# Optimization experiments

Measured on AMD Instinct MI355X. Metric: run time of the kernel, lower is better.

The kernel has to match this reference:

```python
import jax, jax.numpy as jnp
import numpy as np

B, DIM, H, W = 2, 192, 256, 256
WIN = 4
EPS = 1e-5


def _cd_conj(x):
    if len(x) == 1:
        return x
    h = len(x) // 2
    return np.concatenate([_cd_conj(x[:h]), -x[h:]])


def _cd_mult(a, b):
    n = len(a)
    if n == 1:
        return a * b
    h = n // 2
    a1, a2, b1, b2 = a[:h], a[h:], b[:h], b[h:]
    c1 = _cd_mult(a1, b1) - _cd_mult(_cd_conj(b2), a2)
    c2 = _cd_mult(b2, a1) + _cd_mult(a2, _cd_conj(b1))
    return np.concatenate([c1, c2])


def _sedenion_table(n=16):
    # M[i, j, k] = sign s such that e_i * e_j = s * e_k (Cayley-Dickson)
    eye = np.eye(n, dtype=np.float32)
    M = np.zeros((n, n, n), dtype=np.float32)
    for i in range(n):
        for j in range(n):
            M[i, j] = _cd_mult(eye[i], eye[j])
    return M

SED_TABLE = jnp.asarray(_sedenion_table(16))  # (16,16,16)


def layer_norm(x, g, b):
    m = x.mean(-1, keepdims=True)
    v = ((x - m) ** 2).mean(-1, keepdims=True)
    return (x - m) * jax.lax.rsqrt(v + EPS) * g + b


def get_window(x):
    # (B,C,H,W) -> (B,H/4,W/4, s1*s2*C)
    b, c, h, w = x.shape
    x = x.reshape(b, c, h // WIN, WIN, w // WIN, WIN)
    x = x.transpose(0, 2, 4, 3, 5, 1)  # b, h', w', s1, s2, c
    return x.reshape(b, h // WIN, w // WIN, WIN * WIN * c)


def reverse_window(x, c):
    b, hh, ww, _ = x.shape
    x = x.reshape(b, hh, ww, WIN, WIN, c)
    x = x.transpose(0, 5, 1, 3, 2, 4)  # b, c, h', s1, w', s2
    return x.reshape(b, c, hh * WIN, ww * WIN)


def sedenion_full_weight(w_sed):
    # w_sed: (16, dim, dim) component weights -> (16*dim, 16*dim) structured matrix
    d = w_sed.shape[1]
    wf = jnp.einsum('ijk,jde->idke', SED_TABLE, w_sed)
    return wf.reshape(16 * d, 16 * w_sed.shape[2])


def setup_inputs() -> dict:
    key = jax.random.key(0)
    ks = jax.random.split(key, 8)
    d, dh = DIM, 4 * DIM
    s = 0.02
    return {
        'x': jax.random.normal(ks[0], (B, DIM, H, W), jnp.float32),
        'norm1_g': jnp.ones((d,), jnp.float32),
        'norm1_b': jnp.zeros((d,), jnp.float32),
        'w_sed': jax.random.normal(ks[1], (16, d, d), jnp.float32) * s,
        'proj_w': jax.random.normal(ks[2], (d, d), jnp.float32) * s,
        'proj_b': jnp.zeros((d,), jnp.float32),
        'norm2_g': jnp.ones((d,), jnp.float32),
        'norm2_b': jnp.zeros((d,), jnp.float32),
        'fc1_w': jax.random.normal(ks[3], (d, dh), jnp.float32) * s,
        'fc1_b': jnp.zeros((dh,), jnp.float32),
        'fc2_w': jax.random.normal(ks[4], (dh, d), jnp.float32) * s,
        'fc2_b': jnp.zeros((d,), jnp.float32),
    }


def reference(x, norm1_g, norm1_b, w_sed, proj_w, proj_b,
              norm2_g, norm2_b, fc1_w, fc1_b, fc2_w, fc2_b):
    b, c, h, w = x.shape
    # --- attention branch (norm1 -> window -> sedenion linear -> unwindow -> gelu -> proj) ---
    xn = layer_norm(x.transpose(0, 2, 3, 1), norm1_g, norm1_b).transpose(0, 3, 1, 2)
    xw = get_window(xn)                               # (B, H/4, W/4, 16*C)
    wf = sedenion_full_weight(w_sed)                  # (16C, 16C)
    xw = xw @ wf
    x1 = reverse_window(xw, c)                        # (B, C, H, W)
    y = x1.transpose(0, 2, 3, 1)                      # b h w c
    y = jax.nn.gelu(y, approximate=False)
    y = y @ proj_w + proj_b
    x = x + y.transpose(0, 3, 1, 2)
    # --- mlp branch ---
    hbr = layer_norm(x.transpose(0, 2, 3, 1), norm2_g, norm2_b)
    hbr = jax.nn.gelu(hbr @ fc1_w + fc1_b, approximate=False)
    hbr = hbr @ fc2_w + fc2_b
    x = x + hbr.transpose(0, 3, 1, 2)
    return x
```

## Files before the change

### kernel.cpp

```cpp
#include <hip/hip_runtime.h>

typedef short short8 __attribute__((ext_vector_type(8)));
typedef float f32x4 __attribute__((ext_vector_type(4)));

#define DEVINL __device__ __forceinline__

struct SedTab { signed char s[256]; unsigned char j[256]; };

static void cd_mult_host(const float* a, const float* b, float* r, int n) {
    if (n == 1) { r[0] = a[0] * b[0]; return; }
    int h = n / 2;
    float cb1[8], cb2[8], t1[8], t2[8], t3[8], t4[8];
    cb1[0] = b[0]; for (int i = 1; i < h; ++i) cb1[i] = -b[i];
    cb2[0] = b[h]; for (int i = 1; i < h; ++i) cb2[i] = -b[h + i];
    cd_mult_host(a,     b,   t1, h);
    cd_mult_host(cb2,   a+h, t2, h);
    cd_mult_host(b+h,   a,   t3, h);
    cd_mult_host(a+h,   cb1, t4, h);
    for (int i = 0; i < h; ++i) { r[i] = t1[i] - t2[i]; r[h + i] = t3[i] + t4[i]; }
}

static SedTab build_sed() {
    SedTab t{};
    for (int i = 0; i < 16; ++i)
        for (int jj = 0; jj < 16; ++jj) {
            float a[16] = {0}, b[16] = {0}, r[16] = {0};
            a[i] = 1.0f; b[jj] = 1.0f;
            cd_mult_host(a, b, r, 16);
            for (int k = 0; k < 16; ++k)
                if (r[k] != 0.0f) {
                    t.s[i * 16 + k] = (r[k] > 0.f) ? 1 : -1;
                    t.j[i * 16 + k] = (unsigned char)jj;
                }
        }
    return t;
}
static const SedTab g_sed = build_sed();

DEVINL unsigned short f2bf(float v) {
    union { float f; unsigned int u; } c; c.f = v;
    unsigned int r = (c.u + 0x7FFFu + ((c.u >> 16) & 1u)) >> 16;
    return (unsigned short)r;
}
DEVINL float bf2f(unsigned short u) {
    union { unsigned int i; float f; } c; c.i = ((unsigned int)u) << 16; return c.f;
}

DEVINL float gelu_f(float v) {
    float u = 1.5957691216f * (v + 0.044715f * v * v * v);
    return v / (1.0f + __expf(-u));
}

DEVINL void gl2lds16(const void* g, void* l) {
    __builtin_amdgcn_global_load_lds((__attribute__((address_space(1))) const unsigned int*)g,
                                     (__attribute__((address_space(3))) unsigned int*)l, 16, 0, 0);
}

DEVINL int swz(int k, int row) {
    return (k & ~63) | ((((k >> 3) ^ row) & 7) << 3) | (k & 7);
}

__global__ __launch_bounds__(256) void build_wft(const float* __restrict__ w_sed,
                                                 unsigned short* __restrict__ wfT,
                                                 SedTab tab) {
    __shared__ float t[32][33];
    int n0 = blockIdx.y * 32, kk0 = blockIdx.x * 32;
    int k = n0 / 192, i = kk0 / 192;
    int j = tab.j[i * 16 + k];
    float s = (float)tab.s[i * 16 + k];
    int e0 = n0 - k * 192, dd0 = kk0 - i * 192;
    int tx = threadIdx.x & 31, ty = threadIdx.x >> 5;
    const float* base = w_sed + ((size_t)j * 192 + dd0) * 192 + e0;
    for (int it = 0; it < 4; ++it) {
        int row = ty + it * 8;
        t[row][tx] = base[(size_t)row * 192 + tx];
    }
    __syncthreads();
    unsigned short* ob = wfT + (size_t)n0 * 3072 + kk0;
    for (int it = 0; it < 4; ++it) {
        int row = ty + it * 8;
        ob[(size_t)row * 3072 + tx] = f2bf(s * t[tx][row]);
    }
}

__global__ __launch_bounds__(256) void prep_w(const float* __restrict__ proj,
                                              const float* __restrict__ fc1,
                                              const float* __restrict__ fc2,
                                              unsigned short* __restrict__ projT,
                                              unsigned short* __restrict__ fc1T,
                                              unsigned short* __restrict__ fc2T) {
    int t = blockIdx.x * 256 + threadIdx.x;
    if (t < 192 * 192) projT[t] = f2bf(proj[(t % 192) * 192 + t / 192]);
    if (t < 768 * 192) {
        int n = t / 192, k = t % 192;
        fc1T[n * 192 + swz(k, n)] = f2bf(fc1[(size_t)k * 768 + n]);
    }
    if (t < 192 * 768) {
        int o = t / 768, k = t % 768;
        fc2T[o * 768 + swz(k, o)] = f2bf(fc2[(size_t)k * 192 + o]);
    }
}

__global__ __launch_bounds__(256) void ln1_win(const float* __restrict__ x,
                                               const float* __restrict__ g,
                                               const float* __restrict__ bta,
                                               unsigned short* __restrict__ xw,
                                               unsigned short* __restrict__ xwin) {
    __shared__ float vals[192 * 65];
    __shared__ float ps[8][64];
    __shared__ float mrs[2][64];
    int t = threadIdx.x;
    int bid = blockIdx.x;
    int x0 = (bid & 3) << 6;
    int y  = (bid >> 2) & 255;
    int b  = bid >> 10;
    int px = t & 63, cg = t >> 6;
    const float* xp = x + ((size_t)b * 192 * 65536) + (size_t)y * 256 + x0 + px;
    float s = 0.f, s2 = 0.f;
    for (int c = cg; c < 192; c += 4) {
        float v = xp[(size_t)c * 65536];
        vals[c * 65 + px] = v;
        s += v; s2 += v * v;
    }
    ps[cg][px] = s; ps[cg + 4][px] = s2;
    __syncthreads();
    if (t < 64) {
        float S  = ps[0][t] + ps[1][t] + ps[2][t] + ps[3][t];
        float S2 = ps[4][t] + ps[5][t] + ps[6][t] + ps[7][t];
        float mean = S * (1.0f / 192.0f);
        float var  = S2 * (1.0f / 192.0f) - mean * mean;
        mrs[0][t] = mean;
        mrs[1][t] = rsqrtf(var + 1e-5f);
    }
    __syncthreads();
    int wh = y >> 2, wr = y & 3;
    for (int i = t; i < 192 * 64; i += 256) {
        int p = i / 192;
        int c = i - p * 192;
        float v = vals[c * 65 + p];
        int xx = x0 + p;
        int ww = xx >> 2, wc = xx & 3;
        int gp = ((b * 64 + wh) * 64 + ww) * 16 + wr * 4 + wc;
        size_t o = (size_t)gp * 192 + c;
        xwin[o] = f2bf(v);
        xw[o] = f2bf((v - mrs[0][p]) * mrs[1][p] * g[c] + bta[c]);
    }
}

template<int TM, int TN, int EPI>
__global__ __launch_bounds__(256, 2) void gemm_bf16(
        const unsigned short* __restrict__ A, const unsigned short* __restrict__ BT,
        const float* __restrict__ bias, unsigned short* __restrict__ outB,
        unsigned short* __restrict__ xresb,
        const float* __restrict__ g2, const float* __restrict__ b2,
        int K, int N) {
    constexpr int WN = TN / 2;
    constexpr int NT = WN / 16;
    constexpr int MT = TM / 32;
    constexpr int HR = TM / 2;
    __shared__ __align__(16) char smem[(TM * 64 + TN * 64) * 2];
    short* lsA = (short*)smem;
    short* lsB = (short*)(smem + TM * 64 * 2);
    int tid = threadIdx.x, lane = tid & 63, wid = tid >> 6;
    int wrow = wid >> 1, wcol = wid & 1;
    int lm = lane & 15, lq = lane >> 4;
    int bm = blockIdx.x * TM, bn = blockIdx.y * TN;
    const unsigned short* Ag = A + (size_t)bm * K;
    const unsigned short* Bg = BT + (size_t)bn * K;
    f32x4 acc[MT][NT] = {};
    for (int k0 = 0; k0 < K; k0 += 64) {
        #pragma unroll
        for (int it = 0; it < TM / 32; ++it) {
            int p = (it * 4 + wid) * 64 + lane;
            int r = p >> 3;
            int q = (p & 7) ^ (r & 7);
            gl2lds16(Ag + (size_t)r * K + k0 + q * 8, lsA + (it * 4 + wid) * 512);
        }
        #pragma unroll
        for (int it = 0; it < TN / 32; ++it) {
            int p = (it * 4 + wid) * 64 + lane;
            int r = p >> 3;
            int q = (p & 7) ^ (r & 7);
            gl2lds16(Bg + (size_t)r * K + k0 + q * 8, lsB + (it * 4 + wid) * 512);
        }
        __syncthreads();
        #pragma unroll
        for (int s = 0; s < 2; ++s) {
            short8 af[MT], bfr[NT];
            #pragma unroll
            for (int mt = 0; mt < MT; ++mt) {
                int r = wrow * HR + mt * 16 + lm;
                int q = s * 4 + lq;
                int pos = r * 8 + (q ^ (r & 7));
                af[mt] = *(const short8*)&lsA[pos * 8];
            }
            #pragma unroll
            for (int nt = 0; nt < NT; ++nt) {
                int r = wcol * WN + nt * 16 + lm;
                int q = s * 4 + lq;
                int pos = r * 8 + (q ^ (r & 7));
                bfr[nt] = *(const short8*)&lsB[pos * 8];
            }
            #pragma unroll
            for (int mt = 0; mt < MT; ++mt)
                #pragma unroll
                for (int nt = 0; nt < NT; ++nt)
                    acc[mt][nt] = __builtin_amdgcn_mfma_f32_16x16x32_bf16(af[mt], bfr[nt], acc[mt][nt], 0, 0, 0);
        }
        __syncthreads();
    }
    int rowB = bm + wrow * HR + lq * 4;
    int colB = bn + wcol * WN + lm;

    if constexpr (EPI == 0) {
        #pragma unroll
        for (int mt = 0; mt < MT; ++mt)
            #pragma unroll
            for (int nt = 0; nt < NT; ++nt)
                #pragma unroll
                for (int r = 0; r < 4; ++r) {
                    int gr = rowB + mt * 16 + r;
                    int gc = colB + nt * 16;
                    float v = acc[mt][nt][r];
                    if (bias) v += bias[gc];
                    outB[(size_t)gr * N + gc] = f2bf(gelu_f(v));
                }
    } else {
        float sA[MT][4], s2A[MT][4];
        #pragma unroll
        for (int mt = 0; mt < MT; ++mt)
            #pragma unroll
            for (int r = 0; r < 4; ++r) { sA[mt][r] = 0.f; s2A[mt][r] = 0.f; }
        #pragma unroll
        for (int mt = 0; mt < MT; ++mt)
            #pragma unroll
            for (int nt = 0; nt < NT; ++nt)
                #pragma unroll
                for (int r = 0; r < 4; ++r) {
                    int gr = rowB + mt * 16 + r;
                    int gc = colB + nt * 16;
                    size_t o = (size_t)gr * 192 + gc;
                    float v = bf2f(xresb[o]) + acc[mt][nt][r] + bias[gc];
                    xresb[o] = f2bf(v);
                    acc[mt][nt][r] = v;
                    sA[mt][r] += v; s2A[mt][r] += v * v;
                }
        #pragma unroll
        for (int mt = 0; mt < MT; ++mt)
            #pragma unroll
            for (int r = 0; r < 4; ++r)
                #pragma unroll
                for (int msk = 1; msk < 16; msk <<= 1) {
                    sA[mt][r]  += __shfl_xor(sA[mt][r],  msk, 64);
                    s2A[mt][r] += __shfl_xor(s2A[mt][r], msk, 64);
                }
        float* psS   = (float*)smem;
        float* psS2  = psS + 256;
        float* pmean = psS2 + 256;
        float* prsig = pmean + 128;
        if (lm == 0) {
            #pragma unroll
            for (int mt = 0; mt < MT; ++mt)
                #pragma unroll
                for (int r = 0; r < 4; ++r) {
                    int rl = wrow * HR + mt * 16 + lq * 4 + r;
                    psS [rl * 2 + wcol] = sA[mt][r];
                    psS2[rl * 2 + wcol] = s2A[mt][r];
                }
        }
        __syncthreads();
        if (tid < TM) {
            float S  = psS[tid * 2]  + psS[tid * 2 + 1];
            float S2 = psS2[tid * 2] + psS2[tid * 2 + 1];
            float mean = S * (1.0f / 192.0f);
            float var  = S2 * (1.0f / 192.0f) - mean * mean;
            pmean[tid] = mean;
            prsig[tid] = rsqrtf(var + 1e-5f);
        }
        __syncthreads();
        float gw[NT], bw[NT];
        #pragma unroll
        for (int nt = 0; nt < NT; ++nt) {
            int gc = colB + nt * 16;
            gw[nt] = g2[gc]; bw[nt] = b2[gc];
        }
        #pragma unroll
        for (int mt = 0; mt < MT; ++mt)
            #pragma unroll
            for (int nt = 0; nt < NT; ++nt)
                #pragma unroll
                for (int r = 0; r < 4; ++r) {
                    int gr = rowB + mt * 16 + r;
                    int rl = wrow * HR + mt * 16 + lq * 4 + r;
                    int gc = colB + nt * 16;
                    float v = (acc[mt][nt][r] - pmean[rl]) * prsig[rl] * gw[nt] + bw[nt];
                    outB[(size_t)gr * 192 + swz(gc, gr)] = f2bf(v);
                }
    }
}

__global__ __launch_bounds__(256, 2) void ffn_fused(
        const unsigned short* __restrict__ A3, const unsigned short* __restrict__ fc1T,
        const unsigned short* __restrict__ fc2T, const float* __restrict__ b1,
        const float* __restrict__ b2, const unsigned short* __restrict__ xresb,
        float* __restrict__ outF) {
    __shared__ __align__(16) char smem[81920];
    short* A3s = (short*)smem;
    short* wA  = (short*)(smem + 24576);
    short* wB  = (short*)(smem + 49152);
    short* Sb  = (short*)(smem + 73728);
    int tid = threadIdx.x, lane = tid & 63, wid = tid >> 6;
    int wrow = wid >> 1, wcol = wid & 1;
    int lm = lane & 15, lq = lane >> 4;
    int bm = blockIdx.x * 64;

    const unsigned short* A3g = A3 + (size_t)bm * 192;
    #pragma unroll
    for (int it = 0; it < 6; ++it) {
        int ch = (it * 4 + wid) * 64 + lane;
        gl2lds16(A3g + ch * 8, A3s + (it * 4 + wid) * 512);
    }

    f32x4 acc2[2][6] = {};
    for (int nb = 0; nb < 12; ++nb) {
        const unsigned short* f1g = fc1T + (size_t)nb * 64 * 192;
        #pragma unroll
        for (int it = 0; it < 6; ++it) {
            int ch = (it * 4 + wid) * 64 + lane;
            gl2lds16(f1g + ch * 8, wA + (it * 4 + wid) * 512);
        }
        int kb = nb * 64;
        #pragma unroll
        for (int it = 0; it < 6; ++it) {
            int ch = (it * 4 + wid) * 64 + lane;
            gl2lds16(fc2T + (size_t)(ch >> 3) * 768 + kb + (ch & 7) * 8,
                     wB + (it * 4 + wid) * 512);
        }
        __syncthreads();
        f32x4 acc1[2][2] = {};
        #pragma unroll
        for (int ks = 0; ks < 6; ++ks) {
            int c = ks * 4 + lq;
            short8 af[2], bfr[2];
            #pragma unroll
            for (int mt = 0; mt < 2; ++mt) {
                int r = wrow * 32 + mt * 16 + lm;
                int slot = (c & ~7) | ((c ^ r) & 7);
                af[mt] = *(const short8*)&A3s[r * 192 + slot * 8];
            }
            #pragma unroll
            for (int nt = 0; nt < 2; ++nt) {
                int n = wcol * 32 + nt * 16 + lm;
                int slot = (c & ~7) | ((c ^ n) & 7);
                bfr[nt] = *(const short8*)&wA[n * 192 + slot * 8];
            }
            #pragma unroll
            for (int mt = 0; mt < 2; ++mt)
                #pragma unroll
                for (int nt = 0; nt < 2; ++nt)
                    acc1[mt][nt] = __builtin_amdgcn_mfma_f32_16x16x32_bf16(af[mt], bfr[nt], acc1[mt][nt], 0, 0, 0);
        }
        #pragma unroll
        for (int nt = 0; nt < 2; ++nt) {
            int cl = wcol * 32 + nt * 16 + lm;
            float bv = b1[nb * 64 + cl];
            #pragma unroll
            for (int mt = 0; mt < 2; ++mt)
                #pragma unroll
                for (int r = 0; r < 4; ++r) {
                    int row = wrow * 32 + mt * 16 + lq * 4 + r;
                    float v = gelu_f(acc1[mt][nt][r] + bv);
                    int slot = ((cl >> 3) ^ row) & 7;
                    Sb[row * 64 + slot * 8 + (cl & 7)] = f2bf(v);
                }
        }
        __syncthreads();
        #pragma unroll
        for (int ks = 0; ks < 2; ++ks) {
            int c = ks * 4 + lq;
            short8 sf[2], wf[6];
            #pragma unroll
            for (int mt = 0; mt < 2; ++mt) {
                int r = wrow * 32 + mt * 16 + lm;
                int slot = (c ^ r) & 7;
                sf[mt] = *(const short8*)&Sb[r * 64 + slot * 8];
            }
            #pragma unroll
            for (int nt = 0; nt < 6; ++nt) {
                int o = wcol * 96 + nt * 16 + lm;
                int slot = (c ^ o) & 7;
                wf[nt] = *(const short8*)&wB[o * 64 + slot * 8];
            }
            #pragma unroll
            for (int mt = 0; mt < 2; ++mt)
                #pragma unroll
                for (int nt = 0; nt < 6; ++nt)
                    acc2[mt][nt] = __builtin_amdgcn_mfma_f32_16x16x32_bf16(sf[mt], wf[nt], acc2[mt][nt], 0, 0, 0);
        }
        __syncthreads();
    }
    float* T = (float*)smem;
    #pragma unroll
    for (int nt = 0; nt < 6; ++nt) {
        int col = wcol * 96 + nt * 16 + lm;
        float bv = b2[col];
        #pragma unroll
        for (int mt = 0; mt < 2; ++mt)
            #pragma unroll
            for (int r = 0; r < 4; ++r) {
                int row = wrow * 32 + mt * 16 + lq * 4 + r;
                float xr = bf2f(xresb[(size_t)(bm + row) * 192 + col]);
                T[row * 201 + col] = acc2[mt][nt][r] + bv + xr;
            }
    }
    __syncthreads();
    int b  = bm >> 16;
    int wh = (bm >> 10) & 63;
    int ww0 = (bm >> 4) & 63;
    int ybase = wh * 4, xbase = ww0 * 4;
    for (int idx = tid; idx < 3072; idx += 256) {
        int xq = idx & 3, run = idx >> 2;
        int c = run >> 2, wr = run & 3;
        int p = xq * 16 + wr * 4;
        f32x4 val;
        val[0] = T[(p + 0) * 201 + c];
        val[1] = T[(p + 1) * 201 + c];
        val[2] = T[(p + 2) * 201 + c];
        val[3] = T[(p + 3) * 201 + c];
        size_t o = (((size_t)b * 192 + c) * 256 + (ybase + wr)) * 256 + xbase + xq * 4;
        *(f32x4*)&outF[o] = val;
    }
}

extern "C" void kernel_launch(void* const* d_in, const int* in_sizes, int n_in,
                              void* d_out, int out_size, void* d_ws, size_t ws_size,
                              hipStream_t stream) {
    const float* x      = (const float*)d_in[0];
    const float* n1g    = (const float*)d_in[1];
    const float* n1b    = (const float*)d_in[2];
    const float* w_sed  = (const float*)d_in[3];
    const float* proj_w = (const float*)d_in[4];
    const float* proj_b = (const float*)d_in[5];
    const float* n2g    = (const float*)d_in[6];
    const float* n2b    = (const float*)d_in[7];
    const float* fc1_w  = (const float*)d_in[8];
    const float* fc1_b  = (const float*)d_in[9];
    const float* fc2_w  = (const float*)d_in[10];
    const float* fc2_b  = (const float*)d_in[11];
    float* out = (float*)d_out;

    char* ws = (char*)d_ws;
    unsigned short* wfT   = (unsigned short*)(ws);
    unsigned short* xw    = (unsigned short*)(ws + 18874368);
    unsigned short* A2    = (unsigned short*)(ws + 69206016);
    unsigned short* xresb = (unsigned short*)(ws + 119537664);
    unsigned short* projT = (unsigned short*)(ws + 169869312);
    unsigned short* fc1T  = (unsigned short*)(ws + 169943040);
    unsigned short* fc2T  = (unsigned short*)(ws + 170237952);
    unsigned short* A3    = A2;

    build_wft<<<dim3(96, 96), 256, 0, stream>>>(w_sed, wfT, g_sed);
    prep_w<<<576, 256, 0, stream>>>(proj_w, fc1_w, fc2_w, projT, fc1T, fc2T);
    ln1_win<<<2048, 256, 0, stream>>>(x, n1g, n1b, xw, xresb);

    gemm_bf16<128, 128, 0><<<dim3(64, 24), 256, 0, stream>>>(
        xw, wfT, nullptr, A2, nullptr, nullptr, nullptr, 3072, 3072);
    gemm_bf16<128, 192, 3><<<dim3(1024, 1), 256, 0, stream>>>(
        A2, projT, proj_b, A3, xresb, n2g, n2b, 192, 192);
    ffn_fused<<<2048, 256, 0, stream>>>(A3, fc1T, fc2T, fc1_b, fc2_b, xresb, out);
}
```

Measured before the change: 608.4 us.

## Double-buffer fc1 slices and keep A3 tile in registers in fused FFN

The FFN kernel now loads its 64-row activation tile directly from global memory into registers once, rather than staging it in LDS. This frees an LDS region, which is used to double-buffer the fc1 weight slices. fc1 slice nb+2 and fc2 slice nb+1 are now prefetched right after the barriers, so the global-to-LDS copies overlap with the MFMA work of the current slice. The full __syncthreads are replaced by explicit waitcnt plus s_barrier, and s_setprio is raised around the MFMA loops. The cost is more VGPRs for the register-resident A fragments and more delicate hand-written synchronization.

```diff
diff --git a/kernel.cpp b/kernel.cpp
--- a/kernel.cpp
+++ b/kernel.cpp
@@ -305,8 +305,8 @@
         const float* __restrict__ b2, const unsigned short* __restrict__ xresb,
         float* __restrict__ outF) {
     __shared__ __align__(16) char smem[81920];
-    short* A3s = (short*)smem;
-    short* wA  = (short*)(smem + 24576);
+    short* wA0 = (short*)smem;
+    short* wA1 = (short*)(smem + 24576);
     short* wB  = (short*)(smem + 49152);
     short* Sb  = (short*)(smem + 73728);
     int tid = threadIdx.x, lane = tid & 63, wid = tid >> 6;
@@ -315,51 +315,64 @@
     int bm = blockIdx.x * 64;
 
     const unsigned short* A3g = A3 + (size_t)bm * 192;
-    #pragma unroll
-    for (int it = 0; it < 6; ++it) {
-        int ch = (it * 4 + wid) * 64 + lane;
-        gl2lds16(A3g + ch * 8, A3s + (it * 4 + wid) * 512);
-    }
-
-    f32x4 acc2[2][6] = {};
-    for (int nb = 0; nb < 12; ++nb) {
-        const unsigned short* f1g = fc1T + (size_t)nb * 64 * 192;
+
+    auto stage_fc1 = [&](int slice, short* dst) {
+        const unsigned short* f1g = fc1T + (size_t)slice * 64 * 192;
         #pragma unroll
         for (int it = 0; it < 6; ++it) {
             int ch = (it * 4 + wid) * 64 + lane;
-            gl2lds16(f1g + ch * 8, wA + (it * 4 + wid) * 512);
-        }
-        int kb = nb * 64;
+            gl2lds16(f1g + ch * 8, dst + (it * 4 + wid) * 512);
+        }
+    };
+    auto stage_fc2 = [&](int slice) {
+        int kb = slice * 64;
         #pragma unroll
         for (int it = 0; it < 6; ++it) {
             int ch = (it * 4 + wid) * 64 + lane;
             gl2lds16(fc2T + (size_t)(ch >> 3) * 768 + kb + (ch & 7) * 8,
                      wB + (it * 4 + wid) * 512);
         }
-        __syncthreads();
+    };
+
+    stage_fc1(0, wA0);
+    stage_fc1(1, wA1);
+    stage_fc2(0);
+
+    short8 af[6][2];
+    #pragma unroll
+    for (int ks = 0; ks < 6; ++ks) {
+        int c = ks * 4 + lq;
+        #pragma unroll
+        for (int mt = 0; mt < 2; ++mt) {
+            int r = wrow * 32 + mt * 16 + lm;
+            int slot = (c & ~7) | ((c ^ r) & 7);
+            af[ks][mt] = *(const short8*)&A3g[(size_t)r * 192 + slot * 8];
+        }
+    }
+    __syncthreads();
+
+    f32x4 acc2[2][6] = {};
+    for (int nb = 0; nb < 12; ++nb) {
+        const short* wAc = (nb & 1) ? wA1 : wA0;
         f32x4 acc1[2][2] = {};
+        __builtin_amdgcn_s_setprio(1);
         #pragma unroll
         for (int ks = 0; ks < 6; ++ks) {
             int c = ks * 4 + lq;
-            short8 af[2], bfr[2];
-            #pragma unroll
-            for (int mt = 0; mt < 2; ++mt) {
-                int r = wrow * 32 + mt * 16 + lm;
-                int slot = (c & ~7) | ((c ^ r) & 7);
-                af[mt] = *(const short8*)&A3s[r * 192 + slot * 8];
-            }
+            short8 bfr[2];
             #pragma unroll
             for (int nt = 0; nt < 2; ++nt) {
                 int n = wcol * 32 + nt * 16 + lm;
                 int slot = (c & ~7) | ((c ^ n) & 7);
-                bfr[nt] = *(const short8*)&wA[n * 192 + slot * 8];
+                bfr[nt] = *(const short8*)&wAc[n * 192 + slot * 8];
             }
             #pragma unroll
             for (int mt = 0; mt < 2; ++mt)
                 #pragma unroll
                 for (int nt = 0; nt < 2; ++nt)
-                    acc1[mt][nt] = __builtin_amdgcn_mfma_f32_16x16x32_bf16(af[mt], bfr[nt], acc1[mt][nt], 0, 0, 0);
-        }
+                    acc1[mt][nt] = __builtin_amdgcn_mfma_f32_16x16x32_bf16(af[ks][mt], bfr[nt], acc1[mt][nt], 0, 0, 0);
+        }
+        __builtin_amdgcn_s_setprio(0);
         #pragma unroll
         for (int nt = 0; nt < 2; ++nt) {
             int cl = wcol * 32 + nt * 16 + lm;
@@ -374,7 +387,12 @@
                     Sb[row * 64 + slot * 8 + (cl & 7)] = f2bf(v);
                 }
         }
-        __syncthreads();
+        asm volatile("s_waitcnt vmcnt(0) lgkmcnt(0)" ::: "memory");
+        __builtin_amdgcn_sched_barrier(0);
+        __builtin_amdgcn_s_barrier();
+        __builtin_amdgcn_sched_barrier(0);
+        if (nb < 10) stage_fc1(nb + 2, (nb & 1) ? wA1 : wA0);
+        __builtin_amdgcn_s_setprio(1);
         #pragma unroll
         for (int ks = 0; ks < 2; ++ks) {
             int c = ks * 4 + lq;
@@ -397,7 +415,12 @@
                 for (int nt = 0; nt < 6; ++nt)
                     acc2[mt][nt] = __builtin_amdgcn_mfma_f32_16x16x32_bf16(sf[mt], wf[nt], acc2[mt][nt], 0, 0, 0);
         }
-        __syncthreads();
+        __builtin_amdgcn_s_setprio(0);
+        asm volatile("s_waitcnt lgkmcnt(0)" ::: "memory");
+        __builtin_amdgcn_sched_barrier(0);
+        __builtin_amdgcn_s_barrier();
+        __builtin_amdgcn_sched_barrier(0);
+        if (nb < 11) stage_fc2(nb + 1);
     }
     float* T = (float*)smem;
     #pragma unroll
```

New measurement: 582.3 us. 1.04x faster.
